# Kernel optimization log

Measured on AMD Instinct MI355X. Metric: run time of the kernel, lower is better.

Reference implementation:

```python
import jax, jax.numpy as jnp
from jax import lax
import numpy as np

B, K, C = 32, 1024, 256          # batch, num votes, vote feature dim
P, NS, R = 256, 16, 0.3          # num_proposal, nsample, radius
NH, NC, NCLS = 12, 18, 18        # heading bins, size clusters, classes
OUT_CH = 2 + 3 + NH * 2 + NC * 4 + NCLS  # 119
PI = 3.14159265359


def setup_inputs() -> dict:
    key = jax.random.key(0)
    ks = jax.random.split(key, 16)
    d = {}
    d['xyz'] = jax.random.uniform(ks[0], (B, K, 3), dtype=jnp.float32)
    d['features'] = jax.random.normal(ks[1], (B, K, C), dtype=jnp.float32) * 0.1
    d['mean_size_arr'] = jax.random.uniform(ks[2], (NC, 3), dtype=jnp.float32) + 0.5
    cins, couts = [C + 3, 128, 128], [128, 128, 128]
    for i in range(3):
        d[f'w_mlp{i}'] = jax.random.normal(ks[3 + i], (cins[i], couts[i])) / np.sqrt(cins[i]).astype(np.float32)
        d[f'b_mlp{i}'] = jnp.zeros((couts[i],), jnp.float32)
        d[f'g_mlp{i}'] = jnp.ones((couts[i],), jnp.float32)
        d[f'be_mlp{i}'] = jnp.zeros((couts[i],), jnp.float32)
    d['w1'] = jax.random.normal(ks[6], (128, 128)) / np.sqrt(128).astype(np.float32)
    d['b1'] = jnp.zeros((128,), jnp.float32); d['g1'] = jnp.ones((128,), jnp.float32); d['be1'] = jnp.zeros((128,), jnp.float32)
    d['w2'] = jax.random.normal(ks[7], (128, 128)) / np.sqrt(128).astype(np.float32)
    d['b2'] = jnp.zeros((128,), jnp.float32); d['g2'] = jnp.ones((128,), jnp.float32); d['be2'] = jnp.zeros((128,), jnp.float32)
    d['w3'] = jax.random.normal(ks[8], (128, OUT_CH)) / np.sqrt(128).astype(np.float32)
    d['b3'] = jnp.zeros((OUT_CH,), jnp.float32)
    return d


def _fps(xyz):
    # iterative farthest point sampling, start at index 0 (PointNet++ convention)
    def body(carry, _):
        dists, last = carry
        last_pt = jnp.take_along_axis(xyz, last[:, None, None], axis=1)  # (B,1,3)
        d = jnp.sum((xyz - last_pt) ** 2, -1)                             # (B,K)
        dists = jnp.minimum(dists, d)
        nxt = jnp.argmax(dists, -1).astype(jnp.int32)
        return (dists, nxt), nxt
    init = jnp.zeros((B,), jnp.int32)
    dist0 = jnp.full((B, K), 1e10, xyz.dtype)
    (_, _), rest = lax.scan(body, (dist0, init), None, length=P - 1)      # (P-1,B)
    return jnp.concatenate([init[:, None], rest.T], axis=1)               # (B,P)


def _ball_query(xyz, new_xyz):
    # first-NS points within radius R; pad with first valid index
    d2 = jnp.sum((new_xyz[:, :, None, :] - xyz[:, None, :, :]) ** 2, -1)  # (B,P,K)
    cand = jnp.where(d2 < R * R, jnp.arange(K, dtype=jnp.int32)[None, None, :], K)
    srt = jnp.sort(cand, axis=-1)[..., :NS]                               # (B,P,NS)
    first = srt[..., :1]
    idx = jnp.where(srt >= K, first, srt)
    return jnp.minimum(idx, K - 1)


_gather = jax.vmap(lambda a, i: a[i])  # per-batch fancy gather


def reference(xyz, features, mean_size_arr,
              w_mlp0, b_mlp0, g_mlp0, be_mlp0,
              w_mlp1, b_mlp1, g_mlp1, be_mlp1,
              w_mlp2, b_mlp2, g_mlp2, be_mlp2,
              w1, b1, g1, be1, w2, b2, g2, be2, w3, b3):
    inds = _fps(xyz)                                   # (B,P)
    new_xyz = _gather(xyz, inds)                       # (B,P,3) aggregated_vote_xyz
    idx = _ball_query(xyz, new_xyz)                    # (B,P,NS)
    gxyz = (_gather(xyz, idx) - new_xyz[:, :, None, :]) / R   # normalize_xyz=True
    gfeat = _gather(features, idx)                     # (B,P,NS,C)
    x = jnp.concatenate([gxyz, gfeat], -1)             # (B,P,NS,3+C) use_xyz=True
    # SharedMLP: 1x1 conv + BN(inference, identity running stats) + ReLU
    for w, b, g, be in ((w_mlp0, b_mlp0, g_mlp0, be_mlp0),
                        (w_mlp1, b_mlp1, g_mlp1, be_mlp1),
                        (w_mlp2, b_mlp2, g_mlp2, be_mlp2)):
        x = jax.nn.relu(g * (jnp.einsum('bpsc,cd->bpsd', x, w) + b) + be)
    feat = x.max(axis=2)                               # max-pool over nsample -> (B,P,128)
    net = jax.nn.relu6(g1 * (feat @ w1 + b1) + be1)
    net = jax.nn.relu6(g2 * (net @ w2 + b2) + be2)
    net = net @ w3 + b3                                # (B,P,119)
    offset = net[..., :3]
    center = new_xyz + offset
    net = net[..., 3:]                                 # (B,P,116)
    obj = net[:, :, 0:2]
    hs = net[:, :, 2:2 + NH]
    ss = net[:, :, 2 + NH:2 + NH + NC]
    hrn = net[:, :, 2 + NH + NC:2 + 2 * NH + NC]
    hr = hrn * (PI / NH)
    srn = net[:, :, 2 + 2 * NH + NC:2 + 2 * NH + 4 * NC].reshape(B, P, NC, 3)
    sr = srn * mean_size_arr[None, None]
    sem = net[:, :, 2 + 2 * NH + 4 * NC:]
    return (obj, center, hs, hrn, hr, ss, srn, sr, sem, new_xyz, inds)
```

## Files before the change

kernel.cpp:

```cpp
#include <hip/hip_runtime.h>

#define BATCH 32
#define NPTS  1024
#define NFEAT 256
#define NPROP 256
#define NSAMP 16

#define O_OBJ    0
#define O_CENTER 16384
#define O_HS     40960
#define O_HRN    139264
#define O_HR     237568
#define O_SS     335872
#define O_SRN    483328
#define O_SR     925696
#define O_SEM    1368064
#define O_NX     1515520
#define O_INDS   1540096

typedef __attribute__((ext_vector_type(8))) short bf16x8;
typedef __attribute__((ext_vector_type(8))) unsigned short u16x8;
typedef __attribute__((ext_vector_type(2))) float f32x2;
typedef __attribute__((ext_vector_type(16))) float f32x16;

__device__ __forceinline__ unsigned short f2bf(float f) {
  unsigned u = __builtin_bit_cast(unsigned, f);
  u += 0x7fffu + ((u >> 16) & 1u);
  return (unsigned short)(u >> 16);
}

template<int CTRL>
__device__ __forceinline__ float dpp_maxf(float v) {
  int x = __builtin_amdgcn_update_dpp(__builtin_bit_cast(int, v),
          __builtin_bit_cast(int, v), CTRL, 0xf, 0xf, false);
  return fmaxf(v, __builtin_bit_cast(float, x));
}

__global__ __launch_bounds__(256) void fps_prep_kernel(
    const float* __restrict__ xyz,
    const float* __restrict__ feats,
    const float* __restrict__ w0, const float* __restrict__ w1,
    const float* __restrict__ w2, const float* __restrict__ w3,
    const float* __restrict__ b0, const float* __restrict__ g0, const float* __restrict__ be0,
    const float* __restrict__ b1, const float* __restrict__ g1, const float* __restrict__ be1,
    const float* __restrict__ b2, const float* __restrict__ g2, const float* __restrict__ be2,
    const float* __restrict__ wf1, const float* __restrict__ bf1,
    const float* __restrict__ gf1, const float* __restrict__ bef1,
    const float* __restrict__ wf2, const float* __restrict__ bf2,
    const float* __restrict__ gf2, const float* __restrict__ bef2,
    unsigned short* __restrict__ fbf,
    unsigned short* __restrict__ w0bt, unsigned short* __restrict__ w1bt,
    unsigned short* __restrict__ w2bt,
    unsigned short* __restrict__ wfb1, unsigned short* __restrict__ wfb2,
    unsigned short* __restrict__ w3pb,
    float* __restrict__ gb0, float* __restrict__ gb1, float* __restrict__ gb2,
    float* __restrict__ gbf1, float* __restrict__ gbf2,
    float* __restrict__ o_nx,
    float* __restrict__ o_inds)
{
#pragma clang fp contract(off)
  __shared__ float sxyz4[NPTS*4];
  __shared__ int   sInd[NPROP];
  __shared__ unsigned long long sCand[2][4];

  const int tid = threadIdx.x;

  if (blockIdx.x < BATCH) {
    const int b    = blockIdx.x;
    const int wave = tid >> 6;
    const int lane = tid & 63;
    const float* xb = xyz + b * NPTS * 3;
    for (int k = tid; k < NPTS; k += 256) {
      sxyz4[k*4+0] = xb[k*3+0];
      sxyz4[k*4+1] = xb[k*3+1];
      sxyz4[k*4+2] = xb[k*3+2];
    }
    __syncthreads();

    f32x2 px[2], py[2], pz[2], dd[2];
    const int kbase = wave*256 + lane;
#pragma unroll
    for (int a = 0; a < 2; ++a) {
      int k0 = kbase + a*128, k1 = k0 + 64;
      px[a] = (f32x2){sxyz4[k0*4+0], sxyz4[k1*4+0]};
      py[a] = (f32x2){sxyz4[k0*4+1], sxyz4[k1*4+1]};
      pz[a] = (f32x2){sxyz4[k0*4+2], sxyz4[k1*4+2]};
      dd[a] = (f32x2){1e10f, 1e10f};
    }

    int last = 0;
    for (int it = 1; it < NPROP; ++it) {
      float4 lp = *(const float4*)(sxyz4 + last*4);
      f32x2 vlx = (f32x2){lp.x, lp.x};
      f32x2 vly = (f32x2){lp.y, lp.y};
      f32x2 vlz = (f32x2){lp.z, lp.z};
#pragma unroll
      for (int a = 0; a < 2; ++a) {
        f32x2 dx = px[a] - vlx;
        f32x2 dy = py[a] - vly;
        f32x2 dz = pz[a] - vlz;
        f32x2 d  = dx*dx + dy*dy + dz*dz;
        dd[a] = __builtin_elementwise_min(dd[a], d);
      }
      f32x2 mm = __builtin_elementwise_max(dd[0], dd[1]);
      float m = fmaxf(mm[0], mm[1]);
      m = dpp_maxf<0x111>(m);
      m = dpp_maxf<0x112>(m);
      m = dpp_maxf<0x114>(m);
      m = dpp_maxf<0x118>(m);
      m = dpp_maxf<0x142>(m);
      m = dpp_maxf<0x143>(m);
      float gmaxw = __builtin_bit_cast(float,
          __builtin_amdgcn_readlane(__builtin_bit_cast(int, m), 63));
      unsigned long long msk[4];
      msk[0] = __ballot(dd[0][0] == gmaxw);
      msk[1] = __ballot(dd[0][1] == gmaxw);
      msk[2] = __ballot(dd[1][0] == gmaxw);
      msk[3] = __ballot(dd[1][1] == gmaxw);
      int kl = 0;
#pragma unroll
      for (int j = 3; j >= 0; --j) {
        unsigned long long mj = msk[j];
        if (mj) kl = wave*256 + j*64 + (int)__builtin_ctzll(mj);
      }
      if (lane == 0)
        sCand[it & 1][wave] =
            ((unsigned long long)__builtin_bit_cast(unsigned, gmaxw) << 32) |
            (unsigned)(1023 - kl);
      __syncthreads();
      unsigned long long c0 = sCand[it & 1][0];
      unsigned long long c1 = sCand[it & 1][1];
      unsigned long long c2 = sCand[it & 1][2];
      unsigned long long c3 = sCand[it & 1][3];
      unsigned long long w01 = c1 > c0 ? c1 : c0;
      unsigned long long w23 = c3 > c2 ? c3 : c2;
      unsigned long long win = w23 > w01 ? w23 : w01;
      last = 1023 - (int)(unsigned)win;
      if (tid == 0) sInd[it] = last;
    }
    if (tid == 0) sInd[0] = 0;
    __syncthreads();

    for (int s = tid; s < NPROP; s += 256) {
      int ind = sInd[s];
      o_inds[b*NPROP + s] = (float)ind;
      float* nx = o_nx + (b*NPROP + s)*3;
      nx[0] = sxyz4[ind*4+0]; nx[1] = sxyz4[ind*4+1]; nx[2] = sxyz4[ind*4+2];
    }
  } else {
    const int pid = (blockIdx.x - BATCH) * 256 + tid;
    const int PSTRIDE = (256 - BATCH) * 256;
    for (int i = pid; i < (BATCH*NPTS*NFEAT)/8; i += PSTRIDE) {
      size_t o = (size_t)i * 8;
      float4 f0 = *(const float4*)(feats + o);
      float4 f1 = *(const float4*)(feats + o + 4);
      u16x8 v;
      v[0]=f2bf(f0.x); v[1]=f2bf(f0.y); v[2]=f2bf(f0.z); v[3]=f2bf(f0.w);
      v[4]=f2bf(f1.x); v[5]=f2bf(f1.y); v[6]=f2bf(f1.z); v[7]=f2bf(f1.w);
      *(u16x8*)(fbf + o) = v;
    }
    for (int id = pid; id < 119424; id += PSTRIDE) {
      if (id < 36864) {
        int n = id / 288, k = id - 288*n;
        float v = 0.f;
        if (k < 256) v = w0[(k+3)*128 + n];
        else if (k < 259) v = w0[(k-256)*128 + n];
        w0bt[id] = f2bf(v);
      } else if (id < 53248) {
        int j = id - 36864; int n = j >> 7, k = j & 127;
        w1bt[j] = f2bf(w1[k*128 + n]);
      } else if (id < 69632) {
        int j = id - 53248; int n = j >> 7, k = j & 127;
        w2bt[j] = f2bf(w2[k*128 + n]);
      } else if (id < 86016) {
        int j = id - 69632; int n = j >> 7, k = j & 127;
        wfb1[j] = f2bf(wf1[k*128 + n]);
      } else if (id < 102400) {
        int j = id - 86016; int n = j >> 7, k = j & 127;
        wfb2[j] = f2bf(wf2[k*128 + n]);
      } else if (id < 118784) {
        int j = id - 102400; int n = j >> 7, k = j & 127;
        w3pb[j] = (n < 119) ? f2bf(w3[k*119 + n]) : (unsigned short)0;
      } else if (id < 118912) {
        int c = id - 118784; gb0[c] = fmaf(g0[c], b0[c], be0[c]);
      } else if (id < 119040) {
        int c = id - 118912; gb1[c] = fmaf(g1[c], b1[c], be1[c]);
      } else if (id < 119168) {
        int c = id - 119040; gb2[c] = fmaf(g2[c], b2[c], be2[c]);
      } else if (id < 119296) {
        int c = id - 119168; gbf1[c] = fmaf(gf1[c], bf1[c], bef1[c]);
      } else {
        int c = id - 119296; gbf2[c] = fmaf(gf2[c], bf2[c], bef2[c]);
      }
    }
  }
}

__global__ __launch_bounds__(256) void group_mlp_kernel(
    const float* __restrict__ xyz,
    const unsigned short* __restrict__ fbf,
    const unsigned short* __restrict__ w0bt,
    const unsigned short* __restrict__ w1bt,
    const unsigned short* __restrict__ w2bt,
    const float* __restrict__ g0, const float* __restrict__ gb0,
    const float* __restrict__ g1, const float* __restrict__ gb1,
    const float* __restrict__ g2, const float* __restrict__ gb2,
    const float* __restrict__ onx,
    unsigned short* __restrict__ featbf)
{
  __shared__ __align__(16) unsigned short act[4*4096];
  __shared__ int sIdxAll[4][32];

  const int tid  = threadIdx.x;
  const int wave = tid >> 6;
  const int lane = tid & 63;
  const int s  = lane & 31;
  const int h  = lane >> 5;
  const int n0 = s;
  const int gw = blockIdx.x * 4 + wave;
  const int p  = gw * 2 + (s >> 4);
  const int b  = gw >> 7;
  const int samp = s & 15;
  unsigned short* actw = act + wave * 4096;
  int* sIdxW = sIdxAll[wave];

  {
    const float* xb = xyz + b * NPTS * 3;
    const int k0 = lane * 16;
#pragma unroll
    for (int pi = 0; pi < 2; ++pi) {
      const int pp = gw*2 + pi;
      const float qx = onx[pp*3+0];
      const float qy = onx[pp*3+1];
      const float qz = onx[pp*3+2];
      unsigned mask = 0u;
#pragma unroll
      for (int j = 0; j < 16; ++j) {
        int k = k0 + j;
        float dx = __fsub_rn(qx, xb[k*3+0]);
        float dy = __fsub_rn(qy, xb[k*3+1]);
        float dz = __fsub_rn(qz, xb[k*3+2]);
        float d2 = __fadd_rn(__fadd_rn(__fmul_rn(dx,dx), __fmul_rn(dy,dy)), __fmul_rn(dz,dz));
        if (d2 < 0.09f) mask |= (1u << j);
      }
      int cnt  = __popc(mask);
      int incl = cnt;
#pragma unroll
      for (int ofs = 1; ofs < 64; ofs <<= 1) {
        int v = __shfl_up(incl, ofs);
        if (lane >= ofs) incl += v;
      }
      int start = incl - cnt;
      int total = __shfl(incl, 63);
      int fc = mask ? (k0 + __ffs(mask) - 1) : 0x7fffffff;
#pragma unroll
      for (int m = 32; m >= 1; m >>= 1) fc = min(fc, __shfl_xor(fc, m));
      int first = (total > 0) ? fc : (NPTS - 1);
      int* dst = sIdxW + pi*16;
      if (lane >= total && lane < NSAMP) dst[lane] = first;
      int pos = start;
      unsigned mm = mask;
      while (mm && pos < NSAMP) {
        int j = __ffs(mm) - 1; mm &= mm - 1;
        dst[pos] = k0 + j;
        ++pos;
      }
    }
  }
  __syncthreads();

  const int idx = sIdxW[(s>>4)*16 + samp];
  const unsigned short* arow = fbf + ((size_t)(b*NPTS + idx) << 8);

  bf16x8 agx = (bf16x8){0,0,0,0,0,0,0,0};
  if (h == 0) {
    const float* pp = xyz + (size_t)(b*NPTS + idx)*3;
    agx[0] = (short)f2bf((pp[0] - onx[p*3+0]) * (1.0f/0.3f));
    agx[1] = (short)f2bf((pp[1] - onx[p*3+1]) * (1.0f/0.3f));
    agx[2] = (short)f2bf((pp[2] - onx[p*3+2]) * (1.0f/0.3f));
  }

  f32x16 acc[4];
#pragma unroll
  for (int nt = 0; nt < 4; ++nt) acc[nt] = (f32x16)(0.f);

#pragma unroll 4
  for (int ks = 0; ks < 16; ++ks) {
    bf16x8 a = *(const bf16x8*)(arow + ks*16 + h*8);
    const unsigned short* wp = w0bt + (size_t)n0*288 + ks*16 + h*8;
#pragma unroll
    for (int nt = 0; nt < 4; ++nt) {
      bf16x8 bb = *(const bf16x8*)(wp + (size_t)nt*32*288);
      acc[nt] = __builtin_amdgcn_mfma_f32_32x32x16_bf16(a, bb, acc[nt], 0, 0, 0);
    }
  }
  {
    const unsigned short* wp = w0bt + (size_t)n0*288 + 256 + h*8;
#pragma unroll
    for (int nt = 0; nt < 4; ++nt) {
      bf16x8 bb = *(const bf16x8*)(wp + (size_t)nt*32*288);
      acc[nt] = __builtin_amdgcn_mfma_f32_32x32x16_bf16(agx, bb, acc[nt], 0, 0, 0);
    }
  }
#pragma unroll
  for (int nt = 0; nt < 4; ++nt) {
    int c = nt*32 + n0;
    int gch = c >> 3;
    float gg = g0[c], gv = gb0[c];
    int base = gch*256 + (c & 7);
#pragma unroll
    for (int r = 0; r < 16; ++r) {
      int srow = (r & 3) + 8*(r >> 2) + 4*h;
      float v = fmaxf(fmaf(gg, acc[nt][r], gv), 0.f);
      actw[base + ((srow + 2*gch) & 31)*8] = f2bf(v);
    }
  }
  __syncthreads();

#pragma unroll
  for (int nt = 0; nt < 4; ++nt) acc[nt] = (f32x16)(0.f);
#pragma unroll 4
  for (int ks = 0; ks < 8; ++ks) {
    int g = ks*2 + h;
    bf16x8 a = *(const bf16x8*)(actw + g*256 + ((s + 2*g) & 31)*8);
    const unsigned short* wp = w1bt + (size_t)n0*128 + ks*16 + h*8;
#pragma unroll
    for (int nt = 0; nt < 4; ++nt) {
      bf16x8 bb = *(const bf16x8*)(wp + (size_t)nt*32*128);
      acc[nt] = __builtin_amdgcn_mfma_f32_32x32x16_bf16(a, bb, acc[nt], 0, 0, 0);
    }
  }
  __syncthreads();
#pragma unroll
  for (int nt = 0; nt < 4; ++nt) {
    int c = nt*32 + n0;
    int gch = c >> 3;
    float gg = g1[c], gv = gb1[c];
    int base = gch*256 + (c & 7);
#pragma unroll
    for (int r = 0; r < 16; ++r) {
      int srow = (r & 3) + 8*(r >> 2) + 4*h;
      float v = fmaxf(fmaf(gg, acc[nt][r], gv), 0.f);
      actw[base + ((srow + 2*gch) & 31)*8] = f2bf(v);
    }
  }
  __syncthreads();

#pragma unroll
  for (int nt = 0; nt < 4; ++nt) acc[nt] = (f32x16)(0.f);
#pragma unroll 4
  for (int ks = 0; ks < 8; ++ks) {
    int g = ks*2 + h;
    bf16x8 a = *(const bf16x8*)(actw + g*256 + ((s + 2*g) & 31)*8);
    const unsigned short* wp = w2bt + (size_t)n0*128 + ks*16 + h*8;
#pragma unroll
    for (int nt = 0; nt < 4; ++nt) {
      bf16x8 bb = *(const bf16x8*)(wp + (size_t)nt*32*128);
      acc[nt] = __builtin_amdgcn_mfma_f32_32x32x16_bf16(a, bb, acc[nt], 0, 0, 0);
    }
  }
#pragma unroll
  for (int nt = 0; nt < 4; ++nt) {
    int c = nt*32 + n0;
    float gg = g2[c], gv = gb2[c];
    float m0 = 0.f, m1 = 0.f;
#pragma unroll
    for (int r = 0; r < 8; ++r)
      m0 = fmaxf(m0, fmaxf(fmaf(gg, acc[nt][r], gv), 0.f));
#pragma unroll
    for (int r = 8; r < 16; ++r)
      m1 = fmaxf(m1, fmaxf(fmaf(gg, acc[nt][r], gv), 0.f));
    m0 = fmaxf(m0, __shfl_xor(m0, 32));
    m1 = fmaxf(m1, __shfl_xor(m1, 32));
    float vout = h ? m1 : m0;
    featbf[(size_t)(gw*2 + h)*128 + c] = f2bf(vout);
  }
}

__global__ __launch_bounds__(64) void fc_head_kernel(
    const unsigned short* __restrict__ featbf,
    const float* __restrict__ onx,
    const float* __restrict__ msize,
    const unsigned short* __restrict__ wfb1,
    const float* __restrict__ gf1, const float* __restrict__ gbf1,
    const unsigned short* __restrict__ wfb2,
    const float* __restrict__ gf2, const float* __restrict__ gbf2,
    const unsigned short* __restrict__ w3pb,
    const float* __restrict__ b3,
    float* __restrict__ out)
{
  __shared__ __align__(16) unsigned short actw[4096];
  const int lane = threadIdx.x;
  const int s  = lane & 31;
  const int h  = lane >> 5;
  const int n0 = s;
  const int p0 = blockIdx.x * 32;

  f32x16 acc[4];

#pragma unroll
  for (int nt = 0; nt < 4; ++nt) acc[nt] = (f32x16)(0.f);
#pragma unroll
  for (int ks = 0; ks < 8; ++ks) {
    bf16x8 a = *(const bf16x8*)(featbf + (((size_t)(p0 + s)) << 7) + ks*16 + h*8);
    const unsigned short* wp = wfb1 + (size_t)n0*128 + ks*16 + h*8;
#pragma unroll
    for (int nt = 0; nt < 4; ++nt) {
      bf16x8 bb = *(const bf16x8*)(wp + (size_t)nt*32*128);
      acc[nt] = __builtin_amdgcn_mfma_f32_32x32x16_bf16(a, bb, acc[nt], 0, 0, 0);
    }
  }
#pragma unroll
  for (int nt = 0; nt < 4; ++nt) {
    int c = nt*32 + n0;
    int gch = c >> 3;
    float gg = gf1[c], gv = gbf1[c];
    int base = gch*256 + (c & 7);
#pragma unroll
    for (int r = 0; r < 16; ++r) {
      int srow = (r & 3) + 8*(r >> 2) + 4*h;
      float v = fminf(fmaxf(fmaf(gg, acc[nt][r], gv), 0.f), 6.f);
      actw[base + ((srow + 2*gch) & 31)*8] = f2bf(v);
    }
  }

#pragma unroll
  for (int nt = 0; nt < 4; ++nt) acc[nt] = (f32x16)(0.f);
#pragma unroll
  for (int ks = 0; ks < 8; ++ks) {
    int g = ks*2 + h;
    bf16x8 a = *(const bf16x8*)(actw + g*256 + ((s + 2*g) & 31)*8);
    const unsigned short* wp = wfb2 + (size_t)n0*128 + ks*16 + h*8;
#pragma unroll
    for (int nt = 0; nt < 4; ++nt) {
      bf16x8 bb = *(const bf16x8*)(wp + (size_t)nt*32*128);
      acc[nt] = __builtin_amdgcn_mfma_f32_32x32x16_bf16(a, bb, acc[nt], 0, 0, 0);
    }
  }
#pragma unroll
  for (int nt = 0; nt < 4; ++nt) {
    int c = nt*32 + n0;
    int gch = c >> 3;
    float gg = gf2[c], gv = gbf2[c];
    int base = gch*256 + (c & 7);
#pragma unroll
    for (int r = 0; r < 16; ++r) {
      int srow = (r & 3) + 8*(r >> 2) + 4*h;
      float v = fminf(fmaxf(fmaf(gg, acc[nt][r], gv), 0.f), 6.f);
      actw[base + ((srow + 2*gch) & 31)*8] = f2bf(v);
    }
  }

#pragma unroll
  for (int nt = 0; nt < 4; ++nt) acc[nt] = (f32x16)(0.f);
#pragma unroll
  for (int ks = 0; ks < 8; ++ks) {
    int g = ks*2 + h;
    bf16x8 a = *(const bf16x8*)(actw + g*256 + ((s + 2*g) & 31)*8);
    const unsigned short* wp = w3pb + (size_t)n0*128 + ks*16 + h*8;
#pragma unroll
    for (int nt = 0; nt < 4; ++nt) {
      bf16x8 bb = *(const bf16x8*)(wp + (size_t)nt*32*128);
      acc[nt] = __builtin_amdgcn_mfma_f32_32x32x16_bf16(a, bb, acc[nt], 0, 0, 0);
    }
  }
  const float HRC = (float)(3.14159265359 / 12.0);
#pragma unroll
  for (int nt = 0; nt < 4; ++nt) {
    int c = nt*32 + n0;
    if (c >= 119) continue;
    float b3v = b3[c];
#pragma unroll
    for (int r = 0; r < 16; ++r) {
      int srow = (r & 3) + 8*(r >> 2) + 4*h;
      int bp = p0 + srow;
      float v = acc[nt][r] + b3v;
      if (c < 3) {
        out[O_CENTER + bp*3 + c] = onx[bp*3 + c] + v;
      } else if (c < 5) {
        out[O_OBJ + bp*2 + (c-3)] = v;
      } else if (c < 17) {
        out[O_HS + bp*12 + (c-5)] = v;
      } else if (c < 35) {
        out[O_SS + bp*18 + (c-17)] = v;
      } else if (c < 47) {
        int a2 = c - 35;
        out[O_HRN + bp*12 + a2] = v;
        out[O_HR  + bp*12 + a2] = v * HRC;
      } else if (c < 101) {
        int a2 = c - 47;
        out[O_SRN + bp*54 + a2] = v;
        out[O_SR  + bp*54 + a2] = v * msize[a2];
      } else {
        int a2 = c - 101;
        out[O_SEM + bp*18 + a2] = v;
      }
    }
  }
}

extern "C" void kernel_launch(void* const* d_in, const int* in_sizes, int n_in,
                              void* d_out, int out_size, void* d_ws, size_t ws_size,
                              hipStream_t stream) {
  (void)in_sizes; (void)n_in; (void)out_size; (void)ws_size;
  const float* xyz   = (const float*)d_in[0];
  const float* feats = (const float*)d_in[1];
  const float* msize = (const float*)d_in[2];
  const float* w0  = (const float*)d_in[3];
  const float* b0  = (const float*)d_in[4];
  const float* g0  = (const float*)d_in[5];
  const float* be0 = (const float*)d_in[6];
  const float* w1  = (const float*)d_in[7];
  const float* b1  = (const float*)d_in[8];
  const float* g1  = (const float*)d_in[9];
  const float* be1 = (const float*)d_in[10];
  const float* w2  = (const float*)d_in[11];
  const float* b2  = (const float*)d_in[12];
  const float* g2  = (const float*)d_in[13];
  const float* be2 = (const float*)d_in[14];
  const float* wf1  = (const float*)d_in[15];
  const float* bf1  = (const float*)d_in[16];
  const float* gf1  = (const float*)d_in[17];
  const float* bef1 = (const float*)d_in[18];
  const float* wf2  = (const float*)d_in[19];
  const float* bf2  = (const float*)d_in[20];
  const float* gf2  = (const float*)d_in[21];
  const float* bef2 = (const float*)d_in[22];
  const float* w3 = (const float*)d_in[23];
  const float* b3 = (const float*)d_in[24];

  float* out = (float*)d_out;

  char* wsb = (char*)d_ws;
  unsigned short* wfb1   = (unsigned short*)(wsb + 0);
  unsigned short* wfb2   = (unsigned short*)(wsb + 32768);
  unsigned short* w3pb   = (unsigned short*)(wsb + 65536);
  float*          gbf1   = (float*)         (wsb + 98304);
  float*          gbf2   = (float*)         (wsb + 98816);
  unsigned short* fbf    = (unsigned short*)(wsb + 524288);
  unsigned short* featbf = (unsigned short*)(wsb + 17301504);
  unsigned short* w0bt   = (unsigned short*)(wsb + 21495808);
  unsigned short* w1bt   = (unsigned short*)(wsb + 21569536);
  unsigned short* w2bt   = (unsigned short*)(wsb + 21602304);
  float*          gb0    = (float*)         (wsb + 21635072);
  float*          gb1    = (float*)         (wsb + 21635584);
  float*          gb2    = (float*)         (wsb + 21636096);

  fps_prep_kernel<<<256, 256, 0, stream>>>(
      xyz, feats, w0, w1, w2, w3,
      b0, g0, be0, b1, g1, be1, b2, g2, be2,
      wf1, bf1, gf1, bef1, wf2, bf2, gf2, bef2,
      fbf, w0bt, w1bt, w2bt, wfb1, wfb2, w3pb,
      gb0, gb1, gb2, gbf1, gbf2,
      out + O_NX, out + O_INDS);
  group_mlp_kernel<<<(BATCH*NPROP)/8, 256, 0, stream>>>(
      xyz, fbf, w0bt, w1bt, w2bt,
      g0, gb0, g1, gb1, g2, gb2,
      out + O_NX, featbf);
  fc_head_kernel<<<(BATCH*NPROP)/32, 64, 0, stream>>>(
      featbf, out + O_NX, msize,
      wfb1, gf1, gbf1, wfb2, gf2, gbf2, w3pb, b3, out);
}
```

Baseline: 307.6 us.

## Run farthest point sampling in a single wavefront to remove block barriers

The FPS loop now runs in one 64-lane wave per batch instead of four waves. Each lane holds 16 points in registers, and the argmax is resolved entirely with DPP reductions and ballots. This removes the per-iteration __syncthreads and the shared-memory candidate exchange across waves, which are on the serial critical path for 255 iterations. In exchange, each lane does 4x more distance arithmetic per iteration and uses more registers. The other three waves of each FPS block exit early, and the kernel is marked for one block per CU.

```diff
diff --git a/kernel.cpp b/kernel.cpp
--- a/kernel.cpp
+++ b/kernel.cpp
@@ -36,7 +36,7 @@
   return fmaxf(v, __builtin_bit_cast(float, x));
 }
 
-__global__ __launch_bounds__(256) void fps_prep_kernel(
+__global__ __launch_bounds__(256, 1) void fps_prep_kernel(
     const float* __restrict__ xyz,
     const float* __restrict__ feats,
     const float* __restrict__ w0, const float* __restrict__ w1,
@@ -61,31 +61,32 @@
 #pragma clang fp contract(off)
   __shared__ float sxyz4[NPTS*4];
   __shared__ int   sInd[NPROP];
-  __shared__ unsigned long long sCand[2][4];
 
   const int tid = threadIdx.x;
 
   if (blockIdx.x < BATCH) {
-    const int b    = blockIdx.x;
-    const int wave = tid >> 6;
-    const int lane = tid & 63;
+    if (tid >= 64) return;
+    const int b = blockIdx.x;
+    const int t = tid;
     const float* xb = xyz + b * NPTS * 3;
-    for (int k = tid; k < NPTS; k += 256) {
+    for (int k = t; k < NPTS; k += 64) {
       sxyz4[k*4+0] = xb[k*3+0];
       sxyz4[k*4+1] = xb[k*3+1];
       sxyz4[k*4+2] = xb[k*3+2];
     }
-    __syncthreads();
-
-    f32x2 px[2], py[2], pz[2], dd[2];
-    const int kbase = wave*256 + lane;
-#pragma unroll
-    for (int a = 0; a < 2; ++a) {
-      int k0 = kbase + a*128, k1 = k0 + 64;
+
+    f32x2 px[8], py[8], pz[8], dd[8];
+#pragma unroll
+    for (int a = 0; a < 8; ++a) {
+      int k0 = t + 128*a, k1 = k0 + 64;
       px[a] = (f32x2){sxyz4[k0*4+0], sxyz4[k1*4+0]};
       py[a] = (f32x2){sxyz4[k0*4+1], sxyz4[k1*4+1]};
       pz[a] = (f32x2){sxyz4[k0*4+2], sxyz4[k1*4+2]};
       dd[a] = (f32x2){1e10f, 1e10f};
+    }
+#pragma unroll
+    for (int a = 0; a < 8; ++a) {
+      asm volatile("" : "+v"(px[a]), "+v"(py[a]), "+v"(pz[a]));
     }
 
     int last = 0;
@@ -95,14 +96,19 @@
       f32x2 vly = (f32x2){lp.y, lp.y};
       f32x2 vlz = (f32x2){lp.z, lp.z};
 #pragma unroll
-      for (int a = 0; a < 2; ++a) {
+      for (int a = 0; a < 8; ++a) {
         f32x2 dx = px[a] - vlx;
         f32x2 dy = py[a] - vly;
         f32x2 dz = pz[a] - vlz;
         f32x2 d  = dx*dx + dy*dy + dz*dz;
         dd[a] = __builtin_elementwise_min(dd[a], d);
       }
-      f32x2 mm = __builtin_elementwise_max(dd[0], dd[1]);
+      f32x2 m0 = __builtin_elementwise_max(dd[0], dd[1]);
+      f32x2 m1 = __builtin_elementwise_max(dd[2], dd[3]);
+      f32x2 m2 = __builtin_elementwise_max(dd[4], dd[5]);
+      f32x2 m3 = __builtin_elementwise_max(dd[6], dd[7]);
+      f32x2 mm = __builtin_elementwise_max(__builtin_elementwise_max(m0, m1),
+                                           __builtin_elementwise_max(m2, m3));
       float m = fmaxf(mm[0], mm[1]);
       m = dpp_maxf<0x111>(m);
       m = dpp_maxf<0x112>(m);
@@ -110,38 +116,26 @@
       m = dpp_maxf<0x118>(m);
       m = dpp_maxf<0x142>(m);
       m = dpp_maxf<0x143>(m);
-      float gmaxw = __builtin_bit_cast(float,
+      float gmax = __builtin_bit_cast(float,
           __builtin_amdgcn_readlane(__builtin_bit_cast(int, m), 63));
-      unsigned long long msk[4];
-      msk[0] = __ballot(dd[0][0] == gmaxw);
-      msk[1] = __ballot(dd[0][1] == gmaxw);
-      msk[2] = __ballot(dd[1][0] == gmaxw);
-      msk[3] = __ballot(dd[1][1] == gmaxw);
-      int kl = 0;
-#pragma unroll
-      for (int j = 3; j >= 0; --j) {
+      unsigned long long msk[16];
+#pragma unroll
+      for (int a = 0; a < 8; ++a) {
+        msk[2*a]   = __ballot(dd[a][0] == gmax);
+        msk[2*a+1] = __ballot(dd[a][1] == gmax);
+      }
+      int nl = 0;
+#pragma unroll
+      for (int j = 15; j >= 0; --j) {
         unsigned long long mj = msk[j];
-        if (mj) kl = wave*256 + j*64 + (int)__builtin_ctzll(mj);
-      }
-      if (lane == 0)
-        sCand[it & 1][wave] =
-            ((unsigned long long)__builtin_bit_cast(unsigned, gmaxw) << 32) |
-            (unsigned)(1023 - kl);
-      __syncthreads();
-      unsigned long long c0 = sCand[it & 1][0];
-      unsigned long long c1 = sCand[it & 1][1];
-      unsigned long long c2 = sCand[it & 1][2];
-      unsigned long long c3 = sCand[it & 1][3];
-      unsigned long long w01 = c1 > c0 ? c1 : c0;
-      unsigned long long w23 = c3 > c2 ? c3 : c2;
-      unsigned long long win = w23 > w01 ? w23 : w01;
-      last = 1023 - (int)(unsigned)win;
-      if (tid == 0) sInd[it] = last;
-    }
-    if (tid == 0) sInd[0] = 0;
-    __syncthreads();
-
-    for (int s = tid; s < NPROP; s += 256) {
+        if (mj) nl = j*64 + (int)__builtin_ctzll(mj);
+      }
+      last = nl;
+      if (t == 0) sInd[it] = last;
+    }
+    if (t == 0) sInd[0] = 0;
+
+    for (int s = t; s < NPROP; s += 64) {
       int ind = sInd[s];
       o_inds[b*NPROP + s] = (float)ind;
       float* nx = o_nx + (b*NPROP + s)*3;
```

Result: slower. 327.8 us (+6.6%).
